# Kernel tuning notes

Hardware: AMD Instinct MI355X
Metric: run time of the kernel (lower is better)

Reference implementation:

```python
import jax, jax.numpy as jnp
import numpy as np

N = 100000      # nodes
E = 1600000     # edges
D_IN = 128
D_H = 128
D_OUT = 128


def setup_inputs() -> dict:
    key = jax.random.key(0)
    k1, k2, k3, k4, k5, k6 = jax.random.split(key, 6)
    x = jax.random.normal(k1, (N, D_IN), dtype=jnp.float32)
    edge_index = jax.random.randint(k2, (2, E), 0, N, dtype=jnp.int32)
    # GCNConv params: glorot-ish scaled weights, zero bias (PyG default zeros bias)
    W1 = jax.random.normal(k3, (D_IN, D_H), dtype=jnp.float32) * (1.0 / np.sqrt(D_IN))
    b1 = jnp.zeros((D_H,), dtype=jnp.float32)
    W2 = jax.random.normal(k4, (D_H, D_OUT), dtype=jnp.float32) * (1.0 / np.sqrt(D_H))
    b2 = jnpps = jnp.zeros((D_OUT,), dtype=jnp.float32)
    return {"x": x, "edge_index": edge_index, "W1": W1, "b1": b1, "W2": W2, "b2": b2}


def _gcn_layer(x, edge_index, W, b):
    # PyG GCNConv with add_self_loops=True, symmetric normalization:
    # out = D^{-1/2} (A + I) D^{-1/2} (x W) + b, deg computed at target (col)
    n = x.shape[0]
    row, col = edge_index[0], edge_index[1]
    deg = jax.ops.segment_sum(jnp.ones(row.shape, dtype=x.dtype), col,
                              num_segments=n) + 1.0  # +1 for self-loop
    dinv = jax.lax.rsqrt(deg)                         # [N]
    h = x @ W                                         # [N, D_out]
    coef = dinv[row] * dinv[col]                      # [E]
    agg = jax.ops.segment_sum(h[row] * coef[:, None], col, num_segments=n)
    agg = agg + (dinv * dinv)[:, None] * h            # self-loop term
    return agg + b


def reference(x, edge_index, W1, b1, W2, b2):
    h = jax.nn.relu(_gcn_layer(x, edge_index, W1, b1))
    return _gcn_layer(h, edge_index, W2, b2)
```

## Files before the change

kernel.cpp:

```cpp
#include <hip/hip_runtime.h>
#include <hip/hip_bf16.h>

using bf16 = __hip_bfloat16;
typedef __attribute__((ext_vector_type(8))) short short8;
typedef __attribute__((ext_vector_type(4))) float floatx4;

__device__ __forceinline__ float bf2f(unsigned int u) {
    union { unsigned int i; float f; } x; x.i = u << 16; return x.f;
}
__device__ __forceinline__ unsigned short f2bf(float f) {
    union { float f; unsigned int i; } x; x.f = f;
    unsigned int r = x.i + 0x7fffu + ((x.i >> 16) & 1u);
    return (unsigned short)(r >> 16);
}

#define TSHIFT 11
#define TNODES 2048
#define NCHUNK 4096

__global__ __launch_bounds__(256)
void scatter_tiles(const int* __restrict__ row, const int* __restrict__ col,
                   int* __restrict__ tileCur, int* __restrict__ tileBuf,
                   int E, int T, int tcap) {
    __shared__ int grouped[NCHUNK];
    __shared__ int cnt[64], lo[64], off[64], lcur[64];
    const int t = threadIdx.x;
    const int e0 = blockIdx.x * NCHUNK;
    const int valid = min(NCHUNK, E - e0);
    if (t < 64) { cnt[t] = 0; lcur[t] = 0; }
    __syncthreads();
    for (int i = t; i < valid; i += 256)
        atomicAdd(&cnt[(unsigned)col[e0 + i] >> TSHIFT], 1);
    __syncthreads();
    if (t == 0) {
        int run = 0;
        for (int s = 0; s < T; ++s) { lo[s] = run; run += cnt[s]; }
    }
    __syncthreads();
    if (t < T) off[t] = atomicAdd(&tileCur[t], cnt[t]);
    for (int i = t; i < valid; i += 256) {
        int c = col[e0 + i];
        int tl = (unsigned)c >> TSHIFT;
        int slot = lo[tl] + atomicAdd(&lcur[tl], 1);
        grouped[slot] = ((c & (TNODES - 1)) << 17) | row[e0 + i];
    }
    __syncthreads();
    for (int i = t; i < valid; i += 256) {
        int a = 0, b = T - 1;
        while (a < b) { int m = (a + b + 1) >> 1; if (lo[m] <= i) a = m; else b = m - 1; }
        tileBuf[(size_t)a * tcap + off[a] + (i - lo[a])] = grouped[i];
    }
}

__global__ __launch_bounds__(1024)
void build_csr(const int* __restrict__ tileCur, const int* __restrict__ tileBuf,
               int* __restrict__ csr, int* __restrict__ rowptr,
               int* __restrict__ deg64, float* __restrict__ dinv,
               int N, int tcap) {
    __shared__ int deg[TNODES];
    __shared__ int offs[TNODES];
    __shared__ int tsum[1024];
    const int t = threadIdx.x;
    const int tile = blockIdx.x;
    const int nbase = tile << TSHIFT;
    const int cnt = tileCur[tile];
    const int* buf = tileBuf + (size_t)tile * tcap;
    deg[t] = 0; deg[t + 1024] = 0;
    __syncthreads();
    for (int i = t; i < cnt; i += 1024)
        atomicAdd(&deg[buf[i] >> 17], 1);
    __syncthreads();
    const int a0 = deg[2 * t], a1 = deg[2 * t + 1];
    const int s = a0 + a1;
    tsum[t] = s;
    __syncthreads();
    for (int d = 1; d < 1024; d <<= 1) {
        int v = (t >= d) ? tsum[t - d] : 0;
        __syncthreads();
        tsum[t] += v;
        __syncthreads();
    }
    const int tb = tsum[t] - s;
    offs[2 * t] = tb;
    offs[2 * t + 1] = tb + a0;
    const size_t gbase = (size_t)tile * tcap;
    const int n0 = nbase + 2 * t, n1 = n0 + 1;
    if (n0 < N) {
        rowptr[n0] = (int)(gbase + tb);
        deg64[n0] = min(a0, 64);
        dinv[n0] = rsqrtf((float)a0 + 1.0f);
    }
    if (n1 < N) {
        rowptr[n1] = (int)(gbase + tb + a0);
        deg64[n1] = min(a1, 64);
        dinv[n1] = rsqrtf((float)a1 + 1.0f);
    }
    deg[2 * t] = 0; deg[2 * t + 1] = 0;
    __syncthreads();
    for (int i = t; i < cnt; i += 1024) {
        int p = buf[i];
        int ln = p >> 17;
        int pos = offs[ln] + atomicAdd(&deg[ln], 1);
        csr[gbase + pos] = p & 0x1FFFF;
    }
}

__device__ __forceinline__ void store4(float* p, size_t idx, float4 v) {
    *reinterpret_cast<float4*>(p + idx) = v;
}
__device__ __forceinline__ void store4(bf16* p, size_t idx, float4 v) {
    uint2 u;
    u.x = ((unsigned)f2bf(v.y) << 16) | f2bf(v.x);
    u.y = ((unsigned)f2bf(v.w) << 16) | f2bf(v.z);
    *reinterpret_cast<uint2*>(p + idx) = u;
}

template <bool RELU, typename OutT>
__global__ void aggregate(const bf16* __restrict__ xin, const float* __restrict__ dinv,
                          const int* __restrict__ deg64, const int* __restrict__ rowptr,
                          const int* __restrict__ csr,
                          const float* __restrict__ bias, OutT* __restrict__ aggout,
                          int n) {
    const int wave = (blockIdx.x * blockDim.x + threadIdx.x) >> 6;
    const int lane = threadIdx.x & 63;
    if (wave >= n) return;
    const int c = wave;

    const int dg = deg64[c];
    const int base = rowptr[c];
    int idx = 0; float w = 0.f;
    if (lane < dg) {
        idx = csr[base + lane];
        w = dinv[idx];
    }

    const int half = lane >> 5;
    const int sl = lane & 31;
    const bf16* xq = xin + sl * 4;

    float4 acc = make_float4(0.f, 0.f, 0.f, 0.f);
    for (int i = 0; i < dg; i += 16) {
        #pragma unroll
        for (int j = 0; j < 8; ++j) {
            const int e = i + 2 * j + half;
            const int   se = __shfl(idx, e, 64);
            const float we = __shfl(w,   e, 64);
            uint2 u = *reinterpret_cast<const uint2*>(xq + (size_t)se * 128);
            acc.x += bf2f(u.x & 0xffffu) * we;
            acc.y += bf2f(u.x >> 16)     * we;
            acc.z += bf2f(u.y & 0xffffu) * we;
            acc.w += bf2f(u.y >> 16)     * we;
        }
    }
    acc.x += __shfl(acc.x, lane ^ 32, 64);
    acc.y += __shfl(acc.y, lane ^ 32, 64);
    acc.z += __shfl(acc.z, lane ^ 32, 64);
    acc.w += __shfl(acc.w, lane ^ 32, 64);

    if (lane < 32) {
        const float wc = dinv[c];
        uint2 uc = *reinterpret_cast<const uint2*>(xq + (size_t)c * 128);
        float4 bb = *reinterpret_cast<const float4*>(bias + sl * 4);
        float4 r;
        r.x = (acc.x + bf2f(uc.x & 0xffffu) * wc) * wc + bb.x;
        r.y = (acc.y + bf2f(uc.x >> 16)     * wc) * wc + bb.y;
        r.z = (acc.z + bf2f(uc.y & 0xffffu) * wc) * wc + bb.z;
        r.w = (acc.w + bf2f(uc.y >> 16)     * wc) * wc + bb.w;
        if (RELU) {
            r.x = fmaxf(r.x, 0.f); r.y = fmaxf(r.y, 0.f);
            r.z = fmaxf(r.z, 0.f); r.w = fmaxf(r.w, 0.f);
        }
        store4(aggout, (size_t)c * 128 + sl * 4, r);
    }
}

#define WSTR 168
template <typename AT>
__launch_bounds__(256)
__global__ void gemm_mfma(const AT* __restrict__ A, const float* __restrict__ W,
                          bf16* __restrict__ out, int M) {
    __shared__ unsigned short sWt[128 * WSTR];
    __shared__ unsigned short sX[64 * WSTR];
    const int t = threadIdx.x;
    const int row0 = blockIdx.x * 64;

    {
        const int n = t & 127;
        const int kh = (t >> 7) * 4;
        #pragma unroll
        for (int cc = 0; cc < 16; ++cc) {
            const int k0 = cc * 8 + kh;
            float w0 = W[(size_t)(k0 + 0) * 128 + n];
            float w1 = W[(size_t)(k0 + 1) * 128 + n];
            float w2 = W[(size_t)(k0 + 2) * 128 + n];
            float w3 = W[(size_t)(k0 + 3) * 128 + n];
            ushort2 a = make_ushort2(f2bf(w0), f2bf(w1));
            ushort2 b = make_ushort2(f2bf(w2), f2bf(w3));
            *reinterpret_cast<uint2*>(&sWt[n * WSTR + k0]) =
                make_uint2(((unsigned)a.y << 16) | a.x, ((unsigned)b.y << 16) | b.x);
        }
    }
    if constexpr (sizeof(AT) == 4) {
        const float4* Av = reinterpret_cast<const float4*>((const float*)A) + (size_t)row0 * 32;
        #pragma unroll
        for (int i = 0; i < 8; ++i) {
            int idx = t + 256 * i;
            int r = idx >> 5, c4 = (idx & 31) * 4;
            float4 v = make_float4(0.f, 0.f, 0.f, 0.f);
            if (row0 + r < M) v = Av[idx];
            *reinterpret_cast<uint2*>(&sX[r * WSTR + c4]) =
                make_uint2(((unsigned)f2bf(v.y) << 16) | f2bf(v.x),
                           ((unsigned)f2bf(v.w) << 16) | f2bf(v.z));
        }
    } else {
        const uint2* Av = reinterpret_cast<const uint2*>(A) + (size_t)row0 * 32;
        #pragma unroll
        for (int i = 0; i < 8; ++i) {
            int idx = t + 256 * i;
            int r = idx >> 5, c4 = (idx & 31) * 4;
            uint2 u = make_uint2(0u, 0u);
            if (row0 + r < M) u = Av[idx];
            *reinterpret_cast<uint2*>(&sX[r * WSTR + c4]) = u;
        }
    }
    __syncthreads();

    const int wv = t >> 6;
    const int L  = t & 63;
    const int q  = L >> 4;
    const int l16 = L & 15;

    floatx4 acc[8] = {};
    #pragma unroll
    for (int c = 0; c < 4; ++c) {
        short8 a = *reinterpret_cast<const short8*>(&sX[(wv * 16 + l16) * WSTR + c * 32 + q * 8]);
        #pragma unroll
        for (int nt = 0; nt < 8; ++nt) {
            short8 b = *reinterpret_cast<const short8*>(&sWt[(nt * 16 + l16) * WSTR + c * 32 + q * 8]);
            acc[nt] = __builtin_amdgcn_mfma_f32_16x16x32_bf16(a, b, acc[nt], 0, 0, 0);
        }
    }

    __syncthreads();
    unsigned short* sOut = sX;
    #pragma unroll
    for (int nt = 0; nt < 8; ++nt) {
        #pragma unroll
        for (int i = 0; i < 4; ++i) {
            int r = wv * 16 + q * 4 + i;
            sOut[r * 128 + nt * 16 + l16] = f2bf(acc[nt][i]);
        }
    }
    __syncthreads();
    #pragma unroll
    for (int i = 0; i < 4; ++i) {
        int idx = t + 256 * i;
        int r = idx >> 4, c8 = (idx & 15) * 8;
        if (row0 + r < M)
            *reinterpret_cast<uint4*>(out + (size_t)(row0 + r) * 128 + c8) =
                *reinterpret_cast<const uint4*>(&sOut[r * 128 + c8]);
    }
}

extern "C" void kernel_launch(void* const* d_in, const int* in_sizes, int n_in,
                              void* d_out, int out_size, void* d_ws, size_t ws_size,
                              hipStream_t stream) {
    const float* x  = (const float*)d_in[0];
    const int*   ei = (const int*)d_in[1];
    const float* W1 = (const float*)d_in[2];
    const float* b1 = (const float*)d_in[3];
    const float* W2 = (const float*)d_in[4];
    const float* b2 = (const float*)d_in[5];
    float* out = (float*)d_out;

    const int N = in_sizes[0] / 128;
    const int E = in_sizes[1] / 2;
    const int* row = ei;
    const int* col = ei + E;

    const int T = (N + TNODES - 1) >> TSHIFT;
    const int meanT = (E + T - 1) / T;
    const int tcap = meanT + meanT / 8 + 2048;

    char* ws = (char*)d_ws;
    size_t off = 0;
    auto alloc = [&](size_t bytes) {
        void* p = ws + off;
        off += (bytes + 255) & ~(size_t)255;
        return p;
    };
    int*   tileCur = (int*)alloc((size_t)T * 4);
    int*   tileBuf = (int*)alloc((size_t)T * tcap * 4);
    int*   csr     = (int*)alloc((size_t)T * tcap * 4);
    int*   rowptr  = (int*)alloc((size_t)N * 4);
    int*   deg64   = (int*)alloc((size_t)N * 4);
    float* dinv    = (float*)alloc((size_t)N * 4);
    bf16*  ha_bf   = (bf16*)alloc((size_t)N * 128 * 2);
    bf16*  h1_bf   = (bf16*)alloc((size_t)N * 128 * 2);

    hipMemsetAsync(tileCur, 0, (size_t)T * 4, stream);

    scatter_tiles<<<(E + NCHUNK - 1) / NCHUNK, 256, 0, stream>>>(
        row, col, tileCur, tileBuf, E, T, tcap);
    build_csr<<<T, 1024, 0, stream>>>(tileCur, tileBuf, csr, rowptr,
                                      deg64, dinv, N, tcap);

    const int aggBlocks = (int)(((size_t)N * 64 + 255) / 256);
    const int gemmBlocks = (N + 63) / 64;

    gemm_mfma<float><<<gemmBlocks, 256, 0, stream>>>(x, W1, ha_bf, N);
    aggregate<true, bf16><<<aggBlocks, 256, 0, stream>>>(ha_bf, dinv, deg64, rowptr, csr, b1, h1_bf, N);

    gemm_mfma<bf16><<<gemmBlocks, 256, 0, stream>>>(h1_bf, W2, ha_bf, N);
    aggregate<false, float><<<aggBlocks, 256, 0, stream>>>(ha_bf, dinv, deg64, rowptr, csr, b2, out, N);
}
```

Baseline: 340.0 us.

## Use feature-chunked layout with thread-per-node aggregation and prescaled GEMM output

The GEMM now multiplies each output row by dinv[row] and writes it in a chunk-major layout of eight 16-feature slabs per node. Aggregation then maps one thread to one node and one slab, and sums the neighbour rows without per-edge weights or wave shuffles. Each slab-major gather is a contiguous 32-byte read, and each block works on one slab so the gathered data fits in cache. The cost is more per-thread serial loops with divergent degrees, and 16 float accumulators per thread.

```diff
diff --git a/kernel.cpp b/kernel.cpp
--- a/kernel.cpp
+++ b/kernel.cpp
@@ -4,9 +4,14 @@
 using bf16 = __hip_bfloat16;
 typedef __attribute__((ext_vector_type(8))) short short8;
 typedef __attribute__((ext_vector_type(4))) float floatx4;
+typedef __attribute__((ext_vector_type(4))) unsigned int uint4v;
+typedef __attribute__((ext_vector_type(4))) float float4v;
 
 __device__ __forceinline__ float bf2f(unsigned int u) {
     union { unsigned int i; float f; } x; x.i = u << 16; return x.f;
+}
+__device__ __forceinline__ float asf(unsigned int u) {
+    union { unsigned int i; float f; } x; x.i = u; return x.f;
 }
 __device__ __forceinline__ unsigned short f2bf(float f) {
     union { float f; unsigned int i; } x; x.f = f;
@@ -105,72 +110,69 @@
     }
 }
 
-__device__ __forceinline__ void store4(float* p, size_t idx, float4 v) {
-    *reinterpret_cast<float4*>(p + idx) = v;
-}
-__device__ __forceinline__ void store4(bf16* p, size_t idx, float4 v) {
-    uint2 u;
-    u.x = ((unsigned)f2bf(v.y) << 16) | f2bf(v.x);
-    u.y = ((unsigned)f2bf(v.w) << 16) | f2bf(v.z);
-    *reinterpret_cast<uint2*>(p + idx) = u;
-}
-
 template <bool RELU, typename OutT>
-__global__ void aggregate(const bf16* __restrict__ xin, const float* __restrict__ dinv,
-                          const int* __restrict__ deg64, const int* __restrict__ rowptr,
-                          const int* __restrict__ csr,
-                          const float* __restrict__ bias, OutT* __restrict__ aggout,
-                          int n) {
-    const int wave = (blockIdx.x * blockDim.x + threadIdx.x) >> 6;
-    const int lane = threadIdx.x & 63;
-    if (wave >= n) return;
-    const int c = wave;
-
+__global__ __launch_bounds__(256)
+void aggregate(const bf16* __restrict__ xc, const float* __restrict__ dinv,
+               const int* __restrict__ deg64, const int* __restrict__ rowptr,
+               const int* __restrict__ csr, const float* __restrict__ bias,
+               OutT* __restrict__ aggout, int n) {
+    const int chunk = blockIdx.x & 7;
+    const int c = (blockIdx.x >> 3) * 256 + threadIdx.x;
+    if (c >= n) return;
     const int dg = deg64[c];
     const int base = rowptr[c];
-    int idx = 0; float w = 0.f;
-    if (lane < dg) {
-        idx = csr[base + lane];
-        w = dinv[idx];
-    }
-
-    const int half = lane >> 5;
-    const int sl = lane & 31;
-    const bf16* xq = xin + sl * 4;
-
-    float4 acc = make_float4(0.f, 0.f, 0.f, 0.f);
-    for (int i = 0; i < dg; i += 16) {
-        #pragma unroll
-        for (int j = 0; j < 8; ++j) {
-            const int e = i + 2 * j + half;
-            const int   se = __shfl(idx, e, 64);
-            const float we = __shfl(w,   e, 64);
-            uint2 u = *reinterpret_cast<const uint2*>(xq + (size_t)se * 128);
-            acc.x += bf2f(u.x & 0xffffu) * we;
-            acc.y += bf2f(u.x >> 16)     * we;
-            acc.z += bf2f(u.y & 0xffffu) * we;
-            acc.w += bf2f(u.y >> 16)     * we;
-        }
-    }
-    acc.x += __shfl(acc.x, lane ^ 32, 64);
-    acc.y += __shfl(acc.y, lane ^ 32, 64);
-    acc.z += __shfl(acc.z, lane ^ 32, 64);
-    acc.w += __shfl(acc.w, lane ^ 32, 64);
-
-    if (lane < 32) {
-        const float wc = dinv[c];
-        uint2 uc = *reinterpret_cast<const uint2*>(xq + (size_t)c * 128);
-        float4 bb = *reinterpret_cast<const float4*>(bias + sl * 4);
-        float4 r;
-        r.x = (acc.x + bf2f(uc.x & 0xffffu) * wc) * wc + bb.x;
-        r.y = (acc.y + bf2f(uc.x >> 16)     * wc) * wc + bb.y;
-        r.z = (acc.z + bf2f(uc.y & 0xffffu) * wc) * wc + bb.z;
-        r.w = (acc.w + bf2f(uc.y >> 16)     * wc) * wc + bb.w;
-        if (RELU) {
-            r.x = fmaxf(r.x, 0.f); r.y = fmaxf(r.y, 0.f);
-            r.z = fmaxf(r.z, 0.f); r.w = fmaxf(r.w, 0.f);
-        }
-        store4(aggout, (size_t)c * 128 + sl * 4, r);
+    const uint4v* xb = (const uint4v*)(xc + (size_t)chunk * n * 16);
+    float acc[16];
+    #pragma unroll
+    for (int d = 0; d < 16; ++d) acc[d] = 0.f;
+    for (int k = 0; k < dg; ++k) {
+        const int s = csr[base + k];
+        const uint4v a = xb[(size_t)s * 2];
+        const uint4v b = xb[(size_t)s * 2 + 1];
+        #pragma unroll
+        for (int q = 0; q < 4; ++q) {
+            acc[2 * q]     += asf(a[q] << 16);
+            acc[2 * q + 1] += asf(a[q] & 0xffff0000u);
+            acc[8 + 2 * q]     += asf(b[q] << 16);
+            acc[8 + 2 * q + 1] += asf(b[q] & 0xffff0000u);
+        }
+    }
+    {
+        const uint4v a = xb[(size_t)c * 2];
+        const uint4v b = xb[(size_t)c * 2 + 1];
+        #pragma unroll
+        for (int q = 0; q < 4; ++q) {
+            acc[2 * q]     += asf(a[q] << 16);
+            acc[2 * q + 1] += asf(a[q] & 0xffff0000u);
+            acc[8 + 2 * q]     += asf(b[q] << 16);
+            acc[8 + 2 * q + 1] += asf(b[q] & 0xffff0000u);
+        }
+    }
+    const float wc = dinv[c];
+    const float* bb = bias + chunk * 16;
+    float r[16];
+    #pragma unroll
+    for (int d = 0; d < 16; ++d) {
+        r[d] = acc[d] * wc + bb[d];
+        if (RELU) r[d] = fmaxf(r[d], 0.f);
+    }
+    if constexpr (sizeof(OutT) == 2) {
+        uint4v o0, o1;
+        #pragma unroll
+        for (int q = 0; q < 4; ++q) {
+            o0[q] = ((unsigned)f2bf(r[2 * q + 1]) << 16) | f2bf(r[2 * q]);
+            o1[q] = ((unsigned)f2bf(r[8 + 2 * q + 1]) << 16) | f2bf(r[8 + 2 * q]);
+        }
+        uint4v* dst = (uint4v*)((unsigned short*)aggout + ((size_t)chunk * n + c) * 16);
+        __builtin_nontemporal_store(o0, dst);
+        __builtin_nontemporal_store(o1, dst + 1);
+    } else {
+        float4v* dst = (float4v*)((float*)aggout + (size_t)c * 128 + chunk * 16);
+        #pragma unroll
+        for (int q = 0; q < 4; ++q) {
+            float4v v = { r[4 * q], r[4 * q + 1], r[4 * q + 2], r[4 * q + 3] };
+            __builtin_nontemporal_store(v, dst + q);
+        }
     }
 }
 
@@ -178,6 +180,7 @@
 template <typename AT>
 __launch_bounds__(256)
 __global__ void gemm_mfma(const AT* __restrict__ A, const float* __restrict__ W,
+                          const float* __restrict__ dinv,
                           bf16* __restrict__ out, int M) {
     __shared__ unsigned short sWt[128 * WSTR];
     __shared__ unsigned short sX[64 * WSTR];
@@ -213,14 +216,15 @@
                            ((unsigned)f2bf(v.w) << 16) | f2bf(v.z));
         }
     } else {
-        const uint2* Av = reinterpret_cast<const uint2*>(A) + (size_t)row0 * 32;
-        #pragma unroll
-        for (int i = 0; i < 8; ++i) {
+        #pragma unroll
+        for (int i = 0; i < 4; ++i) {
             int idx = t + 256 * i;
-            int r = idx >> 5, c4 = (idx & 31) * 4;
-            uint2 u = make_uint2(0u, 0u);
-            if (row0 + r < M) u = Av[idx];
-            *reinterpret_cast<uint2*>(&sX[r * WSTR + c4]) = u;
+            int c8 = idx >> 7, rr = (idx >> 1) & 63, hh = idx & 1;
+            uint4 u = make_uint4(0u, 0u, 0u, 0u);
+            if (row0 + rr < M)
+                u = *reinterpret_cast<const uint4*>(
+                    (const unsigned short*)A + ((size_t)c8 * M + row0 + rr) * 16 + hh * 8);
+            *reinterpret_cast<uint4*>(&sX[rr * WSTR + c8 * 16 + hh * 8]) = u;
         }
     }
     __syncthreads();
@@ -241,6 +245,12 @@
         }
     }
 
+    float dv[4];
+    #pragma unroll
+    for (int i = 0; i < 4; ++i) {
+        int r = wv * 16 + q * 4 + i;
+        dv[i] = (row0 + r < M) ? dinv[row0 + r] : 1.f;
+    }
     __syncthreads();
     unsigned short* sOut = sX;
     #pragma unroll
@@ -248,17 +258,18 @@
         #pragma unroll
         for (int i = 0; i < 4; ++i) {
             int r = wv * 16 + q * 4 + i;
-            sOut[r * 128 + nt * 16 + l16] = f2bf(acc[nt][i]);
+            sOut[r * 128 + nt * 16 + l16] = f2bf(acc[nt][i] * dv[i]);
         }
     }
     __syncthreads();
     #pragma unroll
     for (int i = 0; i < 4; ++i) {
         int idx = t + 256 * i;
-        int r = idx >> 4, c8 = (idx & 15) * 8;
-        if (row0 + r < M)
-            *reinterpret_cast<uint4*>(out + (size_t)(row0 + r) * 128 + c8) =
-                *reinterpret_cast<const uint4*>(&sOut[r * 128 + c8]);
+        int c8 = idx >> 7, rr = (idx >> 1) & 63, hh = idx & 1;
+        if (row0 + rr < M)
+            *reinterpret_cast<uint4*>(
+                (unsigned short*)out + ((size_t)c8 * M + row0 + rr) * 16 + hh * 8) =
+                *reinterpret_cast<const uint4*>(&sOut[rr * 128 + c8 * 16 + hh * 8]);
     }
 }
 
@@ -305,12 +316,12 @@
     build_csr<<<T, 1024, 0, stream>>>(tileCur, tileBuf, csr, rowptr,
                                       deg64, dinv, N, tcap);
 
-    const int aggBlocks = (int)(((size_t)N * 64 + 255) / 256);
+    const int aggBlocks = 8 * ((N + 255) / 256);
     const int gemmBlocks = (N + 63) / 64;
 
-    gemm_mfma<float><<<gemmBlocks, 256, 0, stream>>>(x, W1, ha_bf, N);
+    gemm_mfma<float><<<gemmBlocks, 256, 0, stream>>>(x, W1, dinv, ha_bf, N);
     aggregate<true, bf16><<<aggBlocks, 256, 0, stream>>>(ha_bf, dinv, deg64, rowptr, csr, b1, h1_bf, N);
 
-    gemm_mfma<bf16><<<gemmBlocks, 256, 0, stream>>>(h1_bf, W2, ha_bf, N);
+    gemm_mfma<bf16><<<gemmBlocks, 256, 0, stream>>>(h1_bf, W2, dinv, ha_bf, N);
     aggregate<false, float><<<aggBlocks, 256, 0, stream>>>(ha_bf, dinv, deg64, rowptr, csr, b2, out, N);
 }
```

After: 580.0 us. +70.6%, slower.

## Fold source dinv scaling into GEMM epilogue and pretranspose weights once

Applied to the files above, without the earlier changes.

Each GEMM output row is pre-scaled by dinv in its epilogue, so the aggregation kernel no longer gathers dinv[idx] per edge or shuffles weights. Invalid lanes point at a zeroed sentinel row N instead. A new prep kernel converts and transposes both weight matrices to bf16 once, so each GEMM block copies them instead of re-converting per block. CSR loads and outputs use nontemporal hints. The trade-offs are an extra bf16 rounding after the dinv multiply and a larger buffer to hold the sentinel row.

```diff
diff --git a/kernel.cpp b/kernel.cpp
--- a/kernel.cpp
+++ b/kernel.cpp
@@ -4,6 +4,8 @@
 using bf16 = __hip_bfloat16;
 typedef __attribute__((ext_vector_type(8))) short short8;
 typedef __attribute__((ext_vector_type(4))) float floatx4;
+typedef __attribute__((ext_vector_type(2))) unsigned int uint2v;
+typedef __attribute__((ext_vector_type(4))) float float4v;
 
 __device__ __forceinline__ float bf2f(unsigned int u) {
     union { unsigned int i; float f; } x; x.i = u << 16; return x.f;
@@ -17,6 +19,17 @@
 #define TSHIFT 11
 #define TNODES 2048
 #define NCHUNK 4096
+
+__global__ __launch_bounds__(256)
+void prep_w(const float* __restrict__ W1, const float* __restrict__ W2,
+            unsigned short* __restrict__ Wt) {
+    const int id = blockIdx.x * 256 + threadIdx.x;
+    const int m = id >> 14;
+    const int r = id & 16383;
+    const int n = r >> 7, k = r & 127;
+    const float* W = m ? W2 : W1;
+    Wt[((size_t)m << 14) + n * 128 + k] = f2bf(W[(size_t)k * 128 + n]);
+}
 
 __global__ __launch_bounds__(256)
 void scatter_tiles(const int* __restrict__ row, const int* __restrict__ col,
@@ -105,16 +118,6 @@
     }
 }
 
-__device__ __forceinline__ void store4(float* p, size_t idx, float4 v) {
-    *reinterpret_cast<float4*>(p + idx) = v;
-}
-__device__ __forceinline__ void store4(bf16* p, size_t idx, float4 v) {
-    uint2 u;
-    u.x = ((unsigned)f2bf(v.y) << 16) | f2bf(v.x);
-    u.y = ((unsigned)f2bf(v.w) << 16) | f2bf(v.z);
-    *reinterpret_cast<uint2*>(p + idx) = u;
-}
-
 template <bool RELU, typename OutT>
 __global__ void aggregate(const bf16* __restrict__ xin, const float* __restrict__ dinv,
                           const int* __restrict__ deg64, const int* __restrict__ rowptr,
@@ -128,11 +131,9 @@
 
     const int dg = deg64[c];
     const int base = rowptr[c];
-    int idx = 0; float w = 0.f;
-    if (lane < dg) {
-        idx = csr[base + lane];
-        w = dinv[idx];
-    }
+    int idx = n;
+    if (lane < dg)
+        idx = __builtin_nontemporal_load(&csr[base + lane]);
 
     const int half = lane >> 5;
     const int sl = lane & 31;
@@ -143,13 +144,12 @@
         #pragma unroll
         for (int j = 0; j < 8; ++j) {
             const int e = i + 2 * j + half;
-            const int   se = __shfl(idx, e, 64);
-            const float we = __shfl(w,   e, 64);
+            const int se = __shfl(idx, e, 64);
             uint2 u = *reinterpret_cast<const uint2*>(xq + (size_t)se * 128);
-            acc.x += bf2f(u.x & 0xffffu) * we;
-            acc.y += bf2f(u.x >> 16)     * we;
-            acc.z += bf2f(u.y & 0xffffu) * we;
-            acc.w += bf2f(u.y >> 16)     * we;
+            acc.x += bf2f(u.x & 0xffffu);
+            acc.y += bf2f(u.x >> 16);
+            acc.z += bf2f(u.y & 0xffffu);
+            acc.w += bf2f(u.y >> 16);
         }
     }
     acc.x += __shfl(acc.x, lane ^ 32, 64);
@@ -162,43 +162,45 @@
         uint2 uc = *reinterpret_cast<const uint2*>(xq + (size_t)c * 128);
         float4 bb = *reinterpret_cast<const float4*>(bias + sl * 4);
         float4 r;
-        r.x = (acc.x + bf2f(uc.x & 0xffffu) * wc) * wc + bb.x;
-        r.y = (acc.y + bf2f(uc.x >> 16)     * wc) * wc + bb.y;
-        r.z = (acc.z + bf2f(uc.y & 0xffffu) * wc) * wc + bb.z;
-        r.w = (acc.w + bf2f(uc.y >> 16)     * wc) * wc + bb.w;
+        r.x = (acc.x + bf2f(uc.x & 0xffffu)) * wc + bb.x;
+        r.y = (acc.y + bf2f(uc.x >> 16))     * wc + bb.y;
+        r.z = (acc.z + bf2f(uc.y & 0xffffu)) * wc + bb.z;
+        r.w = (acc.w + bf2f(uc.y >> 16))     * wc + bb.w;
         if (RELU) {
             r.x = fmaxf(r.x, 0.f); r.y = fmaxf(r.y, 0.f);
             r.z = fmaxf(r.z, 0.f); r.w = fmaxf(r.w, 0.f);
         }
-        store4(aggout, (size_t)c * 128 + sl * 4, r);
+        if constexpr (sizeof(OutT) == 2) {
+            uint2v u;
+            u.x = ((unsigned)f2bf(r.y) << 16) | f2bf(r.x);
+            u.y = ((unsigned)f2bf(r.w) << 16) | f2bf(r.z);
+            __builtin_nontemporal_store(u,
+                (uint2v*)((unsigned short*)aggout + (size_t)c * 128 + sl * 4));
+        } else {
+            float4v v = { r.x, r.y, r.z, r.w };
+            __builtin_nontemporal_store(v,
+                (float4v*)((float*)aggout + (size_t)c * 128 + sl * 4));
+        }
     }
 }
 
 #define WSTR 168
 template <typename AT>
 __launch_bounds__(256)
-__global__ void gemm_mfma(const AT* __restrict__ A, const float* __restrict__ W,
+__global__ void gemm_mfma(const AT* __restrict__ A, const unsigned short* __restrict__ Wt,
+                          const float* __restrict__ dinv,
                           bf16* __restrict__ out, int M) {
     __shared__ unsigned short sWt[128 * WSTR];
     __shared__ unsigned short sX[64 * WSTR];
     const int t = threadIdx.x;
     const int row0 = blockIdx.x * 64;
 
-    {
-        const int n = t & 127;
-        const int kh = (t >> 7) * 4;
-        #pragma unroll
-        for (int cc = 0; cc < 16; ++cc) {
-            const int k0 = cc * 8 + kh;
-            float w0 = W[(size_t)(k0 + 0) * 128 + n];
-            float w1 = W[(size_t)(k0 + 1) * 128 + n];
-            float w2 = W[(size_t)(k0 + 2) * 128 + n];
-            float w3 = W[(size_t)(k0 + 3) * 128 + n];
-            ushort2 a = make_ushort2(f2bf(w0), f2bf(w1));
-            ushort2 b = make_ushort2(f2bf(w2), f2bf(w3));
-            *reinterpret_cast<uint2*>(&sWt[n * WSTR + k0]) =
-                make_uint2(((unsigned)a.y << 16) | a.x, ((unsigned)b.y << 16) | b.x);
-        }
+    #pragma unroll
+    for (int i = 0; i < 8; ++i) {
+        int s = t + 256 * i;
+        int nn = s >> 4, k0 = (s & 15) * 8;
+        *reinterpret_cast<uint4*>(&sWt[nn * WSTR + k0]) =
+            *reinterpret_cast<const uint4*>(&Wt[(size_t)nn * 128 + k0]);
     }
     if constexpr (sizeof(AT) == 4) {
         const float4* Av = reinterpret_cast<const float4*>((const float*)A) + (size_t)row0 * 32;
@@ -241,6 +243,12 @@
         }
     }
 
+    float dv[4];
+    #pragma unroll
+    for (int i = 0; i < 4; ++i) {
+        int r = wv * 16 + q * 4 + i;
+        dv[i] = (row0 + r < M) ? dinv[row0 + r] : 1.f;
+    }
     __syncthreads();
     unsigned short* sOut = sX;
     #pragma unroll
@@ -248,7 +256,7 @@
         #pragma unroll
         for (int i = 0; i < 4; ++i) {
             int r = wv * 16 + q * 4 + i;
-            sOut[r * 128 + nt * 16 + l16] = f2bf(acc[nt][i]);
+            sOut[r * 128 + nt * 16 + l16] = f2bf(acc[nt][i] * dv[i]);
         }
     }
     __syncthreads();
@@ -295,11 +303,14 @@
     int*   rowptr  = (int*)alloc((size_t)N * 4);
     int*   deg64   = (int*)alloc((size_t)N * 4);
     float* dinv    = (float*)alloc((size_t)N * 4);
-    bf16*  ha_bf   = (bf16*)alloc((size_t)N * 128 * 2);
-    bf16*  h1_bf   = (bf16*)alloc((size_t)N * 128 * 2);
+    unsigned short* Wt = (unsigned short*)alloc(2 * 16384 * 2);
+    bf16*  ha_bf   = (bf16*)alloc((size_t)(N + 1) * 128 * 2);
+    bf16*  h1_bf   = (bf16*)alloc((size_t)(N + 1) * 128 * 2);
 
     hipMemsetAsync(tileCur, 0, (size_t)T * 4, stream);
-
+    hipMemsetAsync(ha_bf + (size_t)N * 128, 0, 256, stream);
+
+    prep_w<<<128, 256, 0, stream>>>(W1, W2, Wt);
     scatter_tiles<<<(E + NCHUNK - 1) / NCHUNK, 256, 0, stream>>>(
         row, col, tileCur, tileBuf, E, T, tcap);
     build_csr<<<T, 1024, 0, stream>>>(tileCur, tileBuf, csr, rowptr,
@@ -308,9 +319,9 @@
     const int aggBlocks = (int)(((size_t)N * 64 + 255) / 256);
     const int gemmBlocks = (N + 63) / 64;
 
-    gemm_mfma<float><<<gemmBlocks, 256, 0, stream>>>(x, W1, ha_bf, N);
+    gemm_mfma<float><<<gemmBlocks, 256, 0, stream>>>(x, Wt, dinv, ha_bf, N);
     aggregate<true, bf16><<<aggBlocks, 256, 0, stream>>>(ha_bf, dinv, deg64, rowptr, csr, b1, h1_bf, N);
 
-    gemm_mfma<bf16><<<gemmBlocks, 256, 0, stream>>>(h1_bf, W2, ha_bf, N);
+    gemm_mfma<bf16><<<gemmBlocks, 256, 0, stream>>>(h1_bf, Wt + 16384, dinv, ha_bf, N);
     aggregate<false, float><<<aggBlocks, 256, 0, stream>>>(ha_bf, dinv, deg64, rowptr, csr, b2, out, N);
 }
```

New measurement: 352.5 us. 3.7% more time.
